# Performance work log

Hardware: AMD Instinct MI355X
Metric: run time of the kernel (lower is better)

## Reference

```python
import jax, jax.numpy as jnp
import numpy as np

B, S, D, H = 4, 2048, 1024, 16
DK = D // H

def setup_inputs() -> dict:
    key = jax.random.key(0)
    ks = jax.random.split(key, 8)
    scale = 1.0 / np.sqrt(D)
    q = jax.random.normal(ks[0], (B, S, D), dtype=jnp.float32)
    k = jax.random.normal(ks[1], (B, S, D), dtype=jnp.float32)
    v = jax.random.normal(ks[2], (B, S, D), dtype=jnp.float32)
    # Linear weights stored as [in, out] (applied as x @ W)
    W_q = jax.random.normal(ks[3], (D, D), dtype=jnp.float32) * scale
    W_k = jax.random.normal(ks[4], (D, D), dtype=jnp.float32) * scale
    W_v = jax.random.normal(ks[5], (D, D), dtype=jnp.float32) * scale
    W_o = jax.random.normal(ks[6], (D, D), dtype=jnp.float32) * scale
    mask = jnp.tril(jnp.ones((S, S), dtype=bool))[None, None]  # [1,1,S,S] causal
    return {"q": q, "k": k, "v": v, "W_q": W_q, "W_k": W_k, "W_v": W_v, "W_o": W_o, "mask": mask}

def reference(q, k, v, W_q, W_k, W_v, W_o, mask) -> jnp.ndarray:
    b, sq, _ = q.shape
    sk = k.shape[1]
    # project and split heads: [B,S,D] -> [B,H,S,dk]
    Q = (q @ W_q).reshape(b, sq, H, DK).transpose(0, 2, 1, 3)
    K = (k @ W_k).reshape(b, sk, H, DK).transpose(0, 2, 1, 3)
    V = (v @ W_v).reshape(b, sk, H, DK).transpose(0, 2, 1, 3)
    scores = jnp.einsum('bhqd,bhkd->bhqk', Q, K) / jnp.sqrt(jnp.float32(DK))
    scores = jnp.where(mask, scores, jnp.float32(-1e9))
    attn = jax.nn.softmax(scores, axis=-1)
    out = jnp.einsum('bhqk,bhkd->bhqd', attn, V)  # [B,H,Sq,dk]
    out = out.transpose(0, 2, 1, 3).reshape(b, sq, D)
    return out @ W_o
```

## Files before the change

### kernel.cpp

```cpp
#include <hip/hip_runtime.h>
#include <hip/hip_bf16.h>
#include <stdint.h>

#define B_  4
#define S_  2048
#define D_  1024
#define H_  16
#define DK_ 64
#define M_  (B_*S_)
#define MD_ ((size_t)M_*D_)

typedef unsigned short u16;
typedef unsigned int   u32;
using bh8 = __attribute__((ext_vector_type(8))) short;
using fx4 = __attribute__((ext_vector_type(4))) float;
using us4 = __attribute__((ext_vector_type(4))) unsigned short;

#define C1_ 0.18033688011112042f

__device__ __forceinline__ u16 f2bf(float f){
  union { float f; u32 u; } v; v.f = f;
  u32 r = v.u + 0x7FFFu + ((v.u >> 16) & 1u);
  return (u16)(r >> 16);
}
__device__ __forceinline__ u16 f2bf_fast(float f){
  union { float f; u32 u; } v; v.f = f;
  return (u16)((v.u + 0x8000u) >> 16);
}
__device__ __forceinline__ float fexp2(float x){
  float r;
  asm("v_exp_f32 %0, %1\n\ts_nop 0" : "=v"(r) : "v"(x));
  return r;
}
__device__ __forceinline__ void gl16(const void* g, void* l){
  __builtin_amdgcn_global_load_lds(
      (const __attribute__((address_space(1))) unsigned int*)g,
      (__attribute__((address_space(3))) unsigned int*)l, 16, 0, 0);
}

__device__ __constant__ int QTMAP[16] = {15,14,13,12, 8,9,10,11, 4,5,6,7, 3,2,1,0};

__global__ __launch_bounds__(256) void prep_k(const float* __restrict__ q,
                                              const float* __restrict__ k,
                                              const float* __restrict__ v,
                                              const float* __restrict__ W0,
                                              const float* __restrict__ W1,
                                              const float* __restrict__ W2,
                                              const float* __restrict__ W3,
                                              u16* __restrict__ dq,
                                              u16* __restrict__ dk,
                                              u16* __restrict__ dv,
                                              u16* __restrict__ WT){
  int id = blockIdx.x;
  int tid = threadIdx.x;
  if (id < 12288){
    int z = id >> 12;
    int i = (id & 4095)*256 + tid;
    const float* in = (z==0)? q : (z==1)? k : v;
    u16* out = (z==0)? dq : (z==1)? dk : dv;
    const float4* p = (const float4*)(in + (size_t)i*8);
    float4 a0 = p[0], a1 = p[1];
    u16 o[8];
    o[0]=f2bf(a0.x); o[1]=f2bf(a0.y); o[2]=f2bf(a0.z); o[3]=f2bf(a0.w);
    o[4]=f2bf(a1.x); o[5]=f2bf(a1.y); o[6]=f2bf(a1.z); o[7]=f2bf(a1.w);
    *(bh8*)(out + (size_t)i*8) = *(bh8*)o;
  } else {
    int id2 = id - 12288;
    int z = id2 >> 10, b2 = id2 & 1023;
    int bx = b2 & 31, by = b2 >> 5;
    const float* in = (z==0)? W0 : (z==1)? W1 : (z==2)? W2 : W3;
    float scale = (z==0)? C1_ : 1.0f;
    u16* o = WT + (size_t)z*1024*1024;
    __shared__ u16 tile[32][33];
    int tx = tid & 31, ty = tid >> 5;
    int x0 = bx*32, y0 = by*32;
    #pragma unroll
    for (int j=0;j<32;j+=8) tile[ty+j][tx] = f2bf(in[(size_t)(y0+ty+j)*D_ + x0+tx]*scale);
    __syncthreads();
    #pragma unroll
    for (int j=0;j<32;j+=8) o[(size_t)(x0+ty+j)*D_ + y0+tx] = tile[tx][ty+j];
  }
}

template<int MODE>
__global__ __launch_bounds__(512) void gemm8(const u16* __restrict__ Aqk,
                                             const u16* __restrict__ Av,
                                             const u16* __restrict__ WTb,
                                             u16* __restrict__ Cqk,
                                             u16* __restrict__ VtOut,
                                             float* __restrict__ Cf){
  __shared__ __align__(16) u16 AL[2][128*64];
  __shared__ __align__(16) u16 BL[2][256*64];

  int hbid = blockIdx.x;
  int xcd = hbid & 7, slot = hbid >> 3;
  int pg  = xcd * (MODE==0 ? 24 : 8) + (slot >> 2);
  int x   = slot & 3;
  int y   = (MODE==0) ? (pg & 63) : pg;
  int z   = (MODE==0) ? (pg >> 6) : 0;

  const u16* A  = (MODE==0 && z==2) ? Av : (Aqk + (size_t)z*MD_);
  const u16* BT = WTb + (size_t)z*1024*1024;
  int tid = threadIdx.x;
  int w = tid >> 6, lane = tid & 63, quad = lane >> 4, ln = lane & 15;
  int wm = w >> 2, wn = w & 3;
  int rowBase = y*128, colBase = x*256;

  auto sA = [&](int buf, int kt, int c){
    int s = c*512 + tid;
    int row = s >> 3, kc = (s & 7) ^ (row & 7);
    gl16(&A[(size_t)(rowBase + row)*D_ + kt*64 + kc*8], &AL[buf][s*8]);
  };
  auto sB = [&](int buf, int kt, int c){
    int s = c*512 + tid;
    int row = s >> 3, kc = (s & 7) ^ (row & 7);
    gl16(&BT[(size_t)(colBase + row)*D_ + kt*64 + kc*8], &BL[buf][s*8]);
  };
  auto ridx = [&](int row, int kc){ return row*64 + ((kc ^ (row & 7))*8); };

  fx4 acc[4][4];
  #pragma unroll
  for (int i=0;i<4;i++)
    #pragma unroll
    for (int j=0;j<4;j++) acc[i][j] = (fx4){0.f,0.f,0.f,0.f};

  sA(0,0,0); sA(0,0,1); sB(0,0,0); sB(0,0,1); sB(0,0,2); sB(0,0,3);
  sB(1,1,0); sB(1,1,1); sB(1,1,2);
  asm volatile("s_waitcnt vmcnt(3)" ::: "memory");
  __builtin_amdgcn_s_barrier();

  for (int it = 0; it < 8; ++it){
    int t = 2*it;
    bool h2 = (t+2 < 16), h3 = (t+3 < 16);
    #pragma unroll
    for (int half = 0; half < 2; ++half){
      const u16* Ab = &AL[half][0];
      const u16* Bb = &BL[half][0];

      bh8 bfr[4][2], af0[2][2], af1[2][2];
      #pragma unroll
      for (int n=0;n<4;n++)
        #pragma unroll
        for (int ks=0;ks<2;ks++)
          bfr[n][ks] = *(const bh8*)(&Bb[ridx(wn*64 + n*16 + ln, ks*4+quad)]);
      #pragma unroll
      for (int mi=0;mi<2;mi++)
        #pragma unroll
        for (int ks=0;ks<2;ks++)
          af0[mi][ks] = *(const bh8*)(&Ab[ridx(wm*64 + mi*16 + ln, ks*4+quad)]);
      #pragma unroll
      for (int mi=0;mi<2;mi++)
        #pragma unroll
        for (int ks=0;ks<2;ks++)
          af1[mi][ks] = *(const bh8*)(&Ab[ridx(wm*64 + 32 + mi*16 + ln, ks*4+quad)]);

      if (half == 0){
        sB(1, t+1, 3); sA(1, t+1, 0); sA(1, t+1, 1);
      } else if (h2){
        sB(0, t+2, 3); sA(0, t+2, 0); sA(0, t+2, 1);
      }
      __builtin_amdgcn_s_barrier();
      asm volatile("s_waitcnt lgkmcnt(4)" ::: "memory");
      __builtin_amdgcn_s_setprio(1);
      #pragma unroll
      for (int mi=0;mi<2;mi++)
        #pragma unroll
        for (int n=0;n<4;n++)
          #pragma unroll
          for (int ks=0;ks<2;ks++)
            acc[mi][n] = __builtin_amdgcn_mfma_f32_16x16x32_bf16(
                            af0[mi][ks], bfr[n][ks], acc[mi][n], 0,0,0);
      __builtin_amdgcn_s_setprio(0);
      __builtin_amdgcn_s_barrier();

      if (half == 0){
        if (h2){ sB(0, t+2, 0); sB(0, t+2, 1); sB(0, t+2, 2); }
        if (h2) asm volatile("s_waitcnt vmcnt(3)" ::: "memory");
        else    asm volatile("s_waitcnt vmcnt(0)" ::: "memory");
      } else {
        if (h3){ sB(1, t+3, 0); sB(1, t+3, 1); sB(1, t+3, 2); }
        if (h3) asm volatile("s_waitcnt vmcnt(3)" ::: "memory");
        else    asm volatile("s_waitcnt vmcnt(0)" ::: "memory");
      }
      __builtin_amdgcn_s_barrier();
      asm volatile("s_waitcnt lgkmcnt(0)" ::: "memory");
      __builtin_amdgcn_s_setprio(1);
      #pragma unroll
      for (int mi=0;mi<2;mi++)
        #pragma unroll
        for (int n=0;n<4;n++)
          #pragma unroll
          for (int ks=0;ks<2;ks++)
            acc[2+mi][n] = __builtin_amdgcn_mfma_f32_16x16x32_bf16(
                              af1[mi][ks], bfr[n][ks], acc[2+mi][n], 0,0,0);
      __builtin_amdgcn_s_setprio(0);
      __builtin_amdgcn_s_barrier();
    }
  }

  #pragma unroll
  for (int m=0;m<4;m++){
    int row0 = rowBase + wm*64 + m*16 + quad*4;
    #pragma unroll
    for (int n=0;n<4;n++){
      int col = colBase + wn*64 + n*16 + ln;
      if (MODE == 1){
        #pragma unroll
        for (int r=0;r<4;r++)
          Cf[(size_t)(row0 + r)*D_ + col] = acc[m][n][r];
      } else if (z == 2){
        int bb = row0 >> 11, tok = row0 & (S_-1);
        int hh = col >> 6,  vd  = col & 63;
        us4 pk;
        #pragma unroll
        for (int r=0;r<4;r++) pk[r] = f2bf(acc[m][n][r]);
        *(us4*)&VtOut[((size_t)((bb*16+hh)*64+vd))*S_ + tok] = pk;
      } else {
        #pragma unroll
        for (int r=0;r<4;r++)
          (Cqk + (size_t)z*MD_)[(size_t)(row0 + r)*D_ + col] = f2bf(acc[m][n][r]);
      }
    }
  }
}

__global__ __launch_bounds__(256) void attn_k(const u16* __restrict__ Q,
                                              const u16* __restrict__ Kp,
                                              const u16* __restrict__ VtG,
                                              u16* __restrict__ O){
  __shared__ __align__(16) u16 Kt[2][64*64];
  __shared__ __align__(16) u16 Vt[2][64*64];
  __shared__ __align__(16) u16 Pb[4*16*64];

  int bh = blockIdx.x; int b = bh>>4, h = bh&15;
  int qt = QTMAP[blockIdx.y];
  int tid = threadIdx.x;
  int w = tid >> 6, lane = tid & 63, quad = lane >> 4, ln = lane & 15;
  int q0w = qt*128 + w*32;
  size_t headoff = (size_t)h*DK_;

  bh8 qf[2][2];
  #pragma unroll
  for (int rg=0; rg<2; rg++){
    const u16* qp = Q + (size_t)(b*S_ + q0w + rg*16 + ln)*D_ + headoff + quad*8;
    qf[rg][0] = *(const bh8*)qp;
    qf[rg][1] = *(const bh8*)(qp + 32);
  }

  float m_i[2], l_i[2];
  fx4 oacc[2][4];
  #pragma unroll
  for (int rg=0; rg<2; rg++){
    m_i[rg] = -3e38f; l_i[rg] = 0.f;
    #pragma unroll
    for (int r=0;r<4;r++) oacc[rg][r] = (fx4){0.f,0.f,0.f,0.f};
  }

  auto stage = [&](int k0, int bi){
    #pragma unroll
    for (int i=0;i<2;i++){
      int s = i*256 + tid;
      int n = s >> 3, kc = (s & 7) ^ (n & 7);
      gl16(&Kp[(size_t)(b*S_ + k0 + n)*D_ + headoff + kc*8], &Kt[bi][s*8]);
    }
    #pragma unroll
    for (int i=0;i<2;i++){
      int s = i*256 + tid;
      int vd = s >> 3, c = (s & 7) ^ (vd & 7);
      gl16(&VtG[(size_t)(bh*64 + vd)*S_ + k0 + c*8], &Vt[bi][s*8]);
    }
  };

  u16* Pw = &Pb[w*16*64];
  int ntiles = 2*qt + 2;

  stage(0, 0);
  __syncthreads();

  for (int kt=0; kt<ntiles; kt++){
    int cur = kt & 1;
    if (kt+1 < ntiles) stage((kt+1)*64, cur^1);
    const u16* Kc = Kt[cur];
    const u16* Vc = Vt[cur];
    int k0 = kt*64;
    bool diag = (kt >= 2*qt);

    #pragma unroll
    for (int rg=0; rg<2; rg++){
      fx4 sacc[4];
      __builtin_amdgcn_s_setprio(1);
      #pragma unroll
      for (int t=0;t<4;t++){
        int n = t*16 + ln;
        bh8 kf0 = *(const bh8*)(&Kc[(n*8 + ( quad    ^ (ln&7)))*8]);
        bh8 kf1 = *(const bh8*)(&Kc[(n*8 + ((4+quad) ^ (ln&7)))*8]);
        fx4 zz = (fx4){0.f,0.f,0.f,0.f};
        zz = __builtin_amdgcn_mfma_f32_16x16x32_bf16(kf0, qf[rg][0], zz, 0,0,0);
        zz = __builtin_amdgcn_mfma_f32_16x16x32_bf16(kf1, qf[rg][1], zz, 0,0,0);
        sacc[t] = zz;
      }
      __builtin_amdgcn_s_setprio(0);

      int qg = q0w + rg*16 + ln;
      if (diag){
        #pragma unroll
        for (int t=0;t<4;t++){
          #pragma unroll
          for (int r=0;r<4;r++){
            int kg = k0 + t*16 + quad*4 + r;
            sacc[t][r] = (kg <= qg) ? sacc[t][r] : -3e38f;
          }
        }
      }

      float tm[4];
      #pragma unroll
      for (int t=0;t<4;t++)
        tm[t] = fmaxf(fmaxf(sacc[t][0], sacc[t][1]), fmaxf(sacc[t][2], sacc[t][3]));
      float mloc = fmaxf(fmaxf(tm[0], tm[1]), fmaxf(tm[2], tm[3]));
      mloc = fmaxf(mloc, __shfl_xor(mloc, 16, 64));
      mloc = fmaxf(mloc, __shfl_xor(mloc, 32, 64));

      if (__any(mloc > m_i[rg] + 8.0f)){
        float mn = fmaxf(m_i[rg], mloc);
        float alpha = fexp2(m_i[rg] - mn);
        m_i[rg] = mn;
        l_i[rg] *= alpha;
        float al[4];
        #pragma unroll
        for (int r=0;r<4;r++) al[r] = __shfl(alpha, quad*4 + r, 64);
        #pragma unroll
        for (int vt=0;vt<4;vt++)
          #pragma unroll
          for (int r=0;r<4;r++)
            oacc[rg][vt][r] *= al[r];
      }
      float mn = m_i[rg];

      float ts[4];
      #pragma unroll
      for (int t=0;t<4;t++){
        #pragma unroll
        for (int r=0;r<4;r++) sacc[t][r] = fexp2(sacc[t][r] - mn);
        ts[t] = (sacc[t][0] + sacc[t][1]) + (sacc[t][2] + sacc[t][3]);
      }
      float rs = (ts[0] + ts[1]) + (ts[2] + ts[3]);
      rs += __shfl_xor(rs, 16, 64);
      rs += __shfl_xor(rs, 32, 64);
      l_i[rg] += rs;

      #pragma unroll
      for (int t=0;t<4;t++){
        int hs = (t*4 + quad) ^ (ln & 14);
        us4 pk;
        #pragma unroll
        for (int r=0;r<4;r++) pk[r] = f2bf_fast(sacc[t][r]);
        *(us4*)&Pw[ln*64 + hs*4] = pk;
      }
      asm volatile("s_waitcnt lgkmcnt(0)" ::: "memory");

      __builtin_amdgcn_s_setprio(1);
      #pragma unroll
      for (int s2=0; s2<2; s2++){
        int c = s2*4 + quad;
        int pm = c ^ ((ln>>1) & 7);
        bh8 pf = *(const bh8*)(&Pw[ln*64 + pm*8]);
        #pragma unroll
        for (int vt=0; vt<4; vt++){
          int vd = vt*16 + ln;
          bh8 vf = *(const bh8*)(&Vc[(vd*8 + (c ^ (ln&7)))*8]);
          oacc[rg][vt] = __builtin_amdgcn_mfma_f32_16x16x32_bf16(pf, vf, oacc[rg][vt], 0,0,0);
        }
      }
      __builtin_amdgcn_s_setprio(0);
      asm volatile("s_waitcnt lgkmcnt(0)" ::: "memory");
    }
    __syncthreads();
  }

  #pragma unroll
  for (int rg=0; rg<2; rg++){
    float linv = 1.0f / l_i[rg];
    float lb[4];
    #pragma unroll
    for (int r=0;r<4;r++) lb[r] = __shfl(linv, quad*4 + r, 64);
    #pragma unroll
    for (int r=0;r<4;r++){
      #pragma unroll
      for (int vt=0; vt<4; vt++){
        float ov = oacc[rg][vt][r] * lb[r];
        O[(size_t)(b*S_ + q0w + rg*16 + quad*4 + r)*D_ + headoff + vt*16 + ln] = f2bf(ov);
      }
    }
  }
}

extern "C" void kernel_launch(void* const* d_in, const int* in_sizes, int n_in,
                              void* d_out, int out_size, void* d_ws, size_t ws_size,
                              hipStream_t stream){
  const float* q  = (const float*)d_in[0];
  const float* k  = (const float*)d_in[1];
  const float* v  = (const float*)d_in[2];
  const float* Wq = (const float*)d_in[3];
  const float* Wk = (const float*)d_in[4];
  const float* Wv = (const float*)d_in[5];
  const float* Wo = (const float*)d_in[6];

  u16* ws  = (u16*)d_ws;
  u16* WT  = ws;
  u16* xa  = WT + (size_t)4*1024*1024;
  u16* xb  = xa + MD_;
  u16* Qp  = xb + MD_;
  u16* Kp  = Qp + MD_;

  u16* vb  = (u16*)d_out;
  u16* VtG = vb + MD_;

  prep_k<<<dim3(16384), 256, 0, stream>>>(q, k, v, Wq, Wk, Wv, Wo, xa, xb, vb, WT);

  gemm8<0><<<dim3(768), 512, 0, stream>>>(xa, vb, WT, Qp, VtG, nullptr);

  attn_k<<<dim3(B_*H_, S_/128), 256, 0, stream>>>(Qp, Kp, VtG, Qp);

  gemm8<1><<<dim3(256), 512, 0, stream>>>(Qp, nullptr, WT + (size_t)3*1024*1024,
                                          nullptr, nullptr, (float*)d_out);
}
```

Measured before the change: 326.7 us.

## Interleave QK of second row group with PV of first in attention loop

Splits the per-tile body into QK, softmax, P-write and PV lambdas and reorders them. The QK MFMAs of row group 1 are issued alongside the PV MFMAs of row group 0, so matrix work can overlap the softmax ALU work of the other group. The explicit lgkmcnt waits are replaced by compiler memory barriers, relying on the compiler's own waits for LDS ordering. This holds two score tiles live at once, which raises register pressure and could cut occupancy.

```diff
diff --git a/kernel.cpp b/kernel.cpp
--- a/kernel.cpp
+++ b/kernel.cpp
@@ -274,107 +274,128 @@
   u16* Pw = &Pb[w*16*64];
   int ntiles = 2*qt + 2;
 
+  const u16* Kc; const u16* Vc; int k0; bool diag;
+
+  auto QK = [&](int rg, fx4* sacc){
+    #pragma unroll
+    for (int t=0;t<4;t++){
+      int n = t*16 + ln;
+      bh8 kf0 = *(const bh8*)(&Kc[(n*8 + ( quad    ^ (ln&7)))*8]);
+      bh8 kf1 = *(const bh8*)(&Kc[(n*8 + ((4+quad) ^ (ln&7)))*8]);
+      fx4 zz = (fx4){0.f,0.f,0.f,0.f};
+      zz = __builtin_amdgcn_mfma_f32_16x16x32_bf16(kf0, qf[rg][0], zz, 0,0,0);
+      zz = __builtin_amdgcn_mfma_f32_16x16x32_bf16(kf1, qf[rg][1], zz, 0,0,0);
+      sacc[t] = zz;
+    }
+  };
+
+  auto SM = [&](int rg, fx4* sacc){
+    int qg = q0w + rg*16 + ln;
+    if (diag){
+      #pragma unroll
+      for (int t=0;t<4;t++)
+        #pragma unroll
+        for (int r=0;r<4;r++){
+          int kg = k0 + t*16 + quad*4 + r;
+          sacc[t][r] = (kg <= qg) ? sacc[t][r] : -3e38f;
+        }
+    }
+    float tm[4];
+    #pragma unroll
+    for (int t=0;t<4;t++)
+      tm[t] = fmaxf(fmaxf(sacc[t][0], sacc[t][1]), fmaxf(sacc[t][2], sacc[t][3]));
+    float mloc = fmaxf(fmaxf(tm[0], tm[1]), fmaxf(tm[2], tm[3]));
+    mloc = fmaxf(mloc, __shfl_xor(mloc, 16, 64));
+    mloc = fmaxf(mloc, __shfl_xor(mloc, 32, 64));
+
+    if (__any(mloc > m_i[rg] + 8.0f)){
+      float mn = fmaxf(m_i[rg], mloc);
+      float alpha = fexp2(m_i[rg] - mn);
+      m_i[rg] = mn;
+      l_i[rg] *= alpha;
+      float al[4];
+      #pragma unroll
+      for (int r=0;r<4;r++) al[r] = __shfl(alpha, quad*4 + r, 64);
+      #pragma unroll
+      for (int vt=0;vt<4;vt++)
+        #pragma unroll
+        for (int r=0;r<4;r++)
+          oacc[rg][vt][r] *= al[r];
+    }
+    float mn = m_i[rg];
+    float ts[4];
+    #pragma unroll
+    for (int t=0;t<4;t++){
+      #pragma unroll
+      for (int r=0;r<4;r++) sacc[t][r] = fexp2(sacc[t][r] - mn);
+      ts[t] = (sacc[t][0] + sacc[t][1]) + (sacc[t][2] + sacc[t][3]);
+    }
+    float rs = (ts[0] + ts[1]) + (ts[2] + ts[3]);
+    rs += __shfl_xor(rs, 16, 64);
+    rs += __shfl_xor(rs, 32, 64);
+    l_i[rg] += rs;
+  };
+
+  auto PW = [&](fx4* sacc){
+    #pragma unroll
+    for (int t=0;t<4;t++){
+      int hs = (t*4 + quad) ^ (ln & 14);
+      us4 pk;
+      #pragma unroll
+      for (int r=0;r<4;r++) pk[r] = f2bf_fast(sacc[t][r]);
+      *(us4*)&Pw[ln*64 + hs*4] = pk;
+    }
+  };
+
+  auto PV = [&](int rg){
+    #pragma unroll
+    for (int s2=0; s2<2; s2++){
+      int c = s2*4 + quad;
+      int pm = c ^ ((ln>>1) & 7);
+      bh8 pf = *(const bh8*)(&Pw[ln*64 + pm*8]);
+      #pragma unroll
+      for (int vt=0; vt<4; vt++){
+        int vd = vt*16 + ln;
+        bh8 vf = *(const bh8*)(&Vc[(vd*8 + (c ^ (ln&7)))*8]);
+        oacc[rg][vt] = __builtin_amdgcn_mfma_f32_16x16x32_bf16(pf, vf, oacc[rg][vt], 0,0,0);
+      }
+    }
+  };
+
   stage(0, 0);
   __syncthreads();
 
   for (int kt=0; kt<ntiles; kt++){
     int cur = kt & 1;
     if (kt+1 < ntiles) stage((kt+1)*64, cur^1);
-    const u16* Kc = Kt[cur];
-    const u16* Vc = Vt[cur];
-    int k0 = kt*64;
-    bool diag = (kt >= 2*qt);
-
-    #pragma unroll
-    for (int rg=0; rg<2; rg++){
-      fx4 sacc[4];
-      __builtin_amdgcn_s_setprio(1);
-      #pragma unroll
-      for (int t=0;t<4;t++){
-        int n = t*16 + ln;
-        bh8 kf0 = *(const bh8*)(&Kc[(n*8 + ( quad    ^ (ln&7)))*8]);
-        bh8 kf1 = *(const bh8*)(&Kc[(n*8 + ((4+quad) ^ (ln&7)))*8]);
-        fx4 zz = (fx4){0.f,0.f,0.f,0.f};
-        zz = __builtin_amdgcn_mfma_f32_16x16x32_bf16(kf0, qf[rg][0], zz, 0,0,0);
-        zz = __builtin_amdgcn_mfma_f32_16x16x32_bf16(kf1, qf[rg][1], zz, 0,0,0);
-        sacc[t] = zz;
-      }
-      __builtin_amdgcn_s_setprio(0);
-
-      int qg = q0w + rg*16 + ln;
-      if (diag){
-        #pragma unroll
-        for (int t=0;t<4;t++){
-          #pragma unroll
-          for (int r=0;r<4;r++){
-            int kg = k0 + t*16 + quad*4 + r;
-            sacc[t][r] = (kg <= qg) ? sacc[t][r] : -3e38f;
-          }
-        }
-      }
-
-      float tm[4];
-      #pragma unroll
-      for (int t=0;t<4;t++)
-        tm[t] = fmaxf(fmaxf(sacc[t][0], sacc[t][1]), fmaxf(sacc[t][2], sacc[t][3]));
-      float mloc = fmaxf(fmaxf(tm[0], tm[1]), fmaxf(tm[2], tm[3]));
-      mloc = fmaxf(mloc, __shfl_xor(mloc, 16, 64));
-      mloc = fmaxf(mloc, __shfl_xor(mloc, 32, 64));
-
-      if (__any(mloc > m_i[rg] + 8.0f)){
-        float mn = fmaxf(m_i[rg], mloc);
-        float alpha = fexp2(m_i[rg] - mn);
-        m_i[rg] = mn;
-        l_i[rg] *= alpha;
-        float al[4];
-        #pragma unroll
-        for (int r=0;r<4;r++) al[r] = __shfl(alpha, quad*4 + r, 64);
-        #pragma unroll
-        for (int vt=0;vt<4;vt++)
-          #pragma unroll
-          for (int r=0;r<4;r++)
-            oacc[rg][vt][r] *= al[r];
-      }
-      float mn = m_i[rg];
-
-      float ts[4];
-      #pragma unroll
-      for (int t=0;t<4;t++){
-        #pragma unroll
-        for (int r=0;r<4;r++) sacc[t][r] = fexp2(sacc[t][r] - mn);
-        ts[t] = (sacc[t][0] + sacc[t][1]) + (sacc[t][2] + sacc[t][3]);
-      }
-      float rs = (ts[0] + ts[1]) + (ts[2] + ts[3]);
-      rs += __shfl_xor(rs, 16, 64);
-      rs += __shfl_xor(rs, 32, 64);
-      l_i[rg] += rs;
-
-      #pragma unroll
-      for (int t=0;t<4;t++){
-        int hs = (t*4 + quad) ^ (ln & 14);
-        us4 pk;
-        #pragma unroll
-        for (int r=0;r<4;r++) pk[r] = f2bf_fast(sacc[t][r]);
-        *(us4*)&Pw[ln*64 + hs*4] = pk;
-      }
-      asm volatile("s_waitcnt lgkmcnt(0)" ::: "memory");
-
-      __builtin_amdgcn_s_setprio(1);
-      #pragma unroll
-      for (int s2=0; s2<2; s2++){
-        int c = s2*4 + quad;
-        int pm = c ^ ((ln>>1) & 7);
-        bh8 pf = *(const bh8*)(&Pw[ln*64 + pm*8]);
-        #pragma unroll
-        for (int vt=0; vt<4; vt++){
-          int vd = vt*16 + ln;
-          bh8 vf = *(const bh8*)(&Vc[(vd*8 + (c ^ (ln&7)))*8]);
-          oacc[rg][vt] = __builtin_amdgcn_mfma_f32_16x16x32_bf16(pf, vf, oacc[rg][vt], 0,0,0);
-        }
-      }
-      __builtin_amdgcn_s_setprio(0);
-      asm volatile("s_waitcnt lgkmcnt(0)" ::: "memory");
-    }
+    Kc = Kt[cur];
+    Vc = Vt[cur];
+    k0 = kt*64;
+    diag = (kt >= 2*qt);
+
+    fx4 s0[4], s1[4];
+
+    __builtin_amdgcn_s_setprio(1);
+    QK(0, s0);
+    __builtin_amdgcn_s_setprio(0);
+    SM(0, s0);
+    PW(s0);
+    asm volatile("" ::: "memory");
+
+    __builtin_amdgcn_s_setprio(1);
+    QK(1, s1);
+    PV(0);
+    __builtin_amdgcn_s_setprio(0);
+    asm volatile("" ::: "memory");
+
+    SM(1, s1);
+    PW(s1);
+    asm volatile("" ::: "memory");
+
+    __builtin_amdgcn_s_setprio(1);
+    PV(1);
+    __builtin_amdgcn_s_setprio(0);
+
     __syncthreads();
   }
 
```

Result: slower. 342.1 us (+4.7%).
